# Kernel optimization log

Hardware: AMD Instinct MI355X
Metric: run time of the kernel (lower is better)

Reference implementation:

```python
import jax, jax.numpy as jnp
import numpy as np

NUM_HEADS = 6
ATTN_TH = 0.0
NEG_INF = -10000.0  # masked-score fill for threshold pruning


def setup_inputs() -> dict:
    key = jax.random.key(0)
    k1, k2, k3 = jax.random.split(key, 3)
    B, N, C = 8, 1024, 384
    x = jax.random.normal(k1, (B, N, C), dtype=jnp.float32)
    # Linear weights (torch layout: [out, in]), scaled like default init
    w_qkv = jax.random.normal(k2, (3 * C, C), dtype=jnp.float32) * (1.0 / np.sqrt(C))
    b_qkv = jnp.zeros((3 * C,), dtype=jnp.float32)
    w_proj = jax.random.normal(k3, (C, C), dtype=jnp.float32) * (1.0 / np.sqrt(C))
    b_proj = jnp.zeros((C,), dtype=jnp.float32)
    return {"x": x, "w_qkv": w_qkv, "b_qkv": b_qkv, "w_proj": w_proj, "b_proj": b_proj}


def reference(x, w_qkv, b_qkv, w_proj, b_proj):
    B, N, C = x.shape
    H = NUM_HEADS
    D = C // H
    scale = D ** -0.5
    # QAct nodes are identity (quant=False); QLinear is a plain linear.
    qkv = jnp.einsum('bnc,oc->bno', x, w_qkv) + b_qkv          # [B,N,3C]
    qkv = qkv.reshape(B, N, 3, H, D).transpose(2, 0, 3, 1, 4)   # [3,B,H,N,D]
    q, k, v = qkv[0], qkv[1], qkv[2]
    attn = jnp.einsum('bhnd,bhmd->bhnm', q, k) * scale          # [B,H,N,N]
    # Threshold pruning: scores below Attn_Th are masked out of the softmax.
    attn = jnp.where(attn < ATTN_TH, NEG_INF, attn)
    attn = jax.nn.softmax(attn, axis=-1)
    out = jnp.einsum('bhnm,bhmd->bhnd', attn, v)                # [B,H,N,D]
    out = out.transpose(0, 2, 1, 3).reshape(B, N, C)
    out = jnp.einsum('bnc,oc->bno', out, w_proj) + b_proj
    return out
```

## Files before the change

### kernel.cpp

```cpp
#include <hip/hip_runtime.h>
#include <hip/hip_bf16.h>


typedef __attribute__((__ext_vector_type__(8))) __bf16 bf16x8;
typedef __attribute__((__ext_vector_type__(8))) unsigned short ushort8;
typedef __attribute__((__ext_vector_type__(4))) unsigned short ushort4v;
typedef __attribute__((__ext_vector_type__(4))) short short4v;
typedef __attribute__((__ext_vector_type__(4))) float f32x4;

#define NX 3145728
#define NQ 442368
#define NP 147456

#define QSCALE 0.1803368801111204f

__device__ __forceinline__ f32x4 mfma32(bf16x8 a, bf16x8 b, f32x4 c) {
    return __builtin_amdgcn_mfma_f32_16x16x32_bf16(a, b, c, 0, 0, 0);
}

__device__ __forceinline__ unsigned short f2bf(float f) {
    union { float f; unsigned int i; } x; x.f = f;
    unsigned int u = x.i;
    return (unsigned short)((u + 0x7fffu + ((u >> 16) & 1u)) >> 16);
}

__device__ __forceinline__ unsigned cvtpk(float a, float b) {
    unsigned r;
    asm("v_cvt_pk_bf16_f32 %0, %1, %2" : "=v"(r) : "v"(a), "v"(b));
    return r;
}

__device__ __forceinline__ void dma16(const unsigned short* g, unsigned short* l) {
    __builtin_amdgcn_global_load_lds(
        (const __attribute__((address_space(1))) unsigned int*)g,
        (__attribute__((address_space(3))) unsigned int*)l, 16, 0, 0);
}

__global__ __launch_bounds__(256) void cvt_bf16(
    const float* __restrict__ x, const float* __restrict__ wq, const float* __restrict__ wp,
    unsigned short* __restrict__ xb, unsigned short* __restrict__ wqb, unsigned short* __restrict__ wpb)
{
    int i = blockIdx.x * 256 + threadIdx.x;
    const float* src; unsigned short* dst; int off;
    if (i < NX / 4)              { src = x;  dst = xb;  off = i * 4; }
    else if (i < (NX + NQ) / 4)  { src = wq; dst = wqb; off = i * 4 - NX; }
    else                         { src = wp; dst = wpb; off = i * 4 - NX - NQ; }
    float4 v = *(const float4*)(src + off);
    ushort4v r;
    r[0] = f2bf(v.x); r[1] = f2bf(v.y); r[2] = f2bf(v.z); r[3] = f2bf(v.w);
    *(ushort4v*)(dst + off) = r;
}

template <int MODE, int TM>
__global__ __launch_bounds__(TM * 2) void gemm_bt(
    const unsigned short* __restrict__ A,
    const unsigned short* __restrict__ B,
    const float* __restrict__ bias,
    unsigned short* __restrict__ qg,
    unsigned short* __restrict__ kg,
    unsigned short* __restrict__ vg,
    float* __restrict__ out,
    int M, int N, int K)
{
    const int tid  = threadIdx.x;
    const int lane = tid & 63;
    const int wave = tid >> 6;
    const int l15  = lane & 15;
    const int quad = lane >> 4;
    const int m0 = blockIdx.x * TM;
    const int n0 = blockIdx.y * 128;
    const int wm = (wave >> 1) * 64;
    const int wn = (wave & 1) * 64;

    __shared__ __align__(16) unsigned short As[2 * TM * 32];
    __shared__ __align__(16) unsigned short Bs[2 * 128 * 32];

    f32x4 acc[4][4];
    #pragma unroll
    for (int i = 0; i < 4; ++i)
        #pragma unroll
        for (int j = 0; j < 4; ++j)
            acc[i][j] = (f32x4){0.f, 0.f, 0.f, 0.f};

    auto stage = [&](int k0, int buf) {
        #pragma unroll
        for (int t = 0; t < 2; ++t) {
            int i = tid + t * TM * 2;
            dma16(A + (size_t)(m0 + (i >> 2)) * K + k0 + (i & 3) * 8,
                  As + buf * TM * 32 + t * TM * 16 + wave * 512);
        }
        #pragma unroll
        for (int t = 0; t < 512 / (TM * 2); ++t) {
            int i = tid + t * TM * 2;
            dma16(B + (size_t)(n0 + (i >> 2)) * K + k0 + (i & 3) * 8,
                  Bs + buf * 4096 + t * TM * 16 + wave * 512);
        }
    };

    const int nk = K >> 5;
    stage(0, 0);
    for (int ki = 0; ki < nk; ++ki) {
        __syncthreads();
        if (ki + 1 < nk) stage((ki + 1) << 5, (ki + 1) & 1);
        const unsigned short* as = As + (ki & 1) * TM * 32;
        const unsigned short* bs = Bs + (ki & 1) * 4096;

        bf16x8 af[4], bff[4];
        #pragma unroll
        for (int mt = 0; mt < 4; ++mt)
            af[mt] = *(const bf16x8*)(as + (wm + mt * 16 + l15) * 32 + quad * 8);
        #pragma unroll
        for (int nt = 0; nt < 4; ++nt)
            bff[nt] = *(const bf16x8*)(bs + (wn + nt * 16 + l15) * 32 + quad * 8);
        #pragma unroll
        for (int mt = 0; mt < 4; ++mt)
            #pragma unroll
            for (int nt = 0; nt < 4; ++nt)
                acc[mt][nt] = mfma32(af[mt], bff[nt], acc[mt][nt]);
    }

    if constexpr (MODE == 0) {
        if (n0 < 384) {
            #pragma unroll
            for (int nt = 0; nt < 4; ++nt) {
                int n = n0 + wn + nt * 16 + l15;
                float bv = bias[n];
                #pragma unroll
                for (int mt = 0; mt < 4; ++mt) {
                    int mbase = m0 + wm + mt * 16 + quad * 4;
                    #pragma unroll
                    for (int r = 0; r < 4; ++r)
                        qg[(size_t)(mbase + r) * 384 + n] = f2bf((acc[mt][nt][r] + bv) * QSCALE);
                }
            }
        } else if (n0 < 768) {
            #pragma unroll
            for (int nt = 0; nt < 4; ++nt) {
                int n = n0 + wn + nt * 16 + l15;
                float bv = bias[n];
                int c2 = n - 384;
                int h = c2 >> 6, ck = c2 & 63;
                int half = ck >> 5, qd = (ck >> 3) & 3, j = ck & 7;
                #pragma unroll
                for (int mt = 0; mt < 4; ++mt) {
                    int mbase = m0 + wm + mt * 16 + quad * 4;
                    #pragma unroll
                    for (int r = 0; r < 4; ++r) {
                        int tok = mbase + r;
                        int b = tok >> 10, kv = tok & 1023;
                        int kt = kv >> 4, lk = kv & 15;
                        kg[(size_t)(b * 6 + h) * 65536 +
                           ((((size_t)kt * 2 + half) * 4 + qd) * 16 + lk) * 8 + j]
                            = f2bf(acc[mt][nt][r] + bv);
                    }
                }
            }
        } else {
            #pragma unroll
            for (int nt = 0; nt < 4; ++nt) {
                int n = n0 + wn + nt * 16 + l15;
                float bv = bias[n];
                int c2 = n - 768;
                int h = c2 >> 6, d = c2 & 63;
                int dt = d >> 4, lv = d & 15;
                #pragma unroll
                for (int mt = 0; mt < 4; ++mt) {
                    int mbase = m0 + wm + mt * 16 + quad * 4;
                    int b = mbase >> 10, kvb = mbase & 1023;
                    int cc = kvb >> 6;
                    int hh = (kvb >> 5) & 1;
                    int rem2 = kvb & 31;
                    int qv, j;
                    if (rem2 < 16) { qv = (rem2 >> 3) << 1; j = rem2 & 7; }
                    else {
                        int m2 = rem2 - 16;
                        qv = 1 + ((m2 >> 3) << 1);
                        j = (((m2 >> 2) & 1) ^ 1) << 2;
                    }
                    ushort4v pk;
                    #pragma unroll
                    for (int r = 0; r < 4; ++r) pk[r] = f2bf(acc[mt][nt][r] + bv);
                    *(ushort4v*)(vg + (size_t)(b * 6 + h) * 65536 +
                                 ((((size_t)cc * 2 + hh) * 4 + dt) * 4 + qv) * 128 + lv * 8 + j) = pk;
                }
            }
        }
    } else {
        #pragma unroll
        for (int nt = 0; nt < 4; ++nt) {
            int n = n0 + wn + nt * 16 + l15;
            float bv = bias[n];
            #pragma unroll
            for (int mt = 0; mt < 4; ++mt) {
                int mbase = m0 + wm + mt * 16 + quad * 4;
                #pragma unroll
                for (int r = 0; r < 4; ++r)
                    out[(size_t)(mbase + r) * N + n] = acc[mt][nt][r] + bv;
            }
        }
    }
}

__global__ __launch_bounds__(256) void attn_fused(
    const unsigned short* __restrict__ qg,
    const unsigned short* __restrict__ kg,
    const unsigned short* __restrict__ vg,
    unsigned short* __restrict__ aout)
{
    const int tid  = threadIdx.x;
    const int wave = tid >> 6;
    const int lane = tid & 63;
    const int l15  = lane & 15;
    const int quad = lane >> 4;
    const int id = blockIdx.x;
    const int s  = id % 48;
    const int qt = id / 48;
    const int b  = s / 6;
    const int h  = s % 6;

    const size_t rowbase = (size_t)b * 1024;
    const unsigned short* Kslab = kg + (size_t)s * 65536;
    const unsigned short* Vslab = vg + (size_t)s * 65536;
    const int q0 = qt * 64 + wave * 16;

    __shared__ __align__(16) unsigned short Kb[2 * 4096];
    __shared__ __align__(16) unsigned short Vb[2 * 4096];

    bf16x8 aq0, aq1;
    {
        const unsigned short* qrow = qg + (rowbase + q0 + l15) * 384 + h * 64 + quad * 8;
        aq0 = *(const bf16x8*)qrow;
        aq1 = *(const bf16x8*)(qrow + 32);
    }

    union { unsigned short us[8]; bf16x8 v; } ones_u;
    #pragma unroll
    for (int i = 0; i < 8; ++i) ones_u.us[i] = 0x3F80;
    const bf16x8 ONES8 = ones_u.v;

    f32x4 accO[4];
    #pragma unroll
    for (int dt = 0; dt < 4; ++dt) accO[dt] = (f32x4){0.f, 0.f, 0.f, 0.f};
    f32x4 accS = (f32x4){0.f, 0.f, 0.f, 0.f};

    auto stage = [&](int c, int buf) {
        #pragma unroll
        for (int t = 0; t < 2; ++t) {
            int i = tid + t * 256;
            dma16(Kslab + (size_t)c * 4096 + i * 8, Kb + buf * 4096 + t * 2048 + wave * 512);
            dma16(Vslab + (size_t)c * 4096 + i * 8, Vb + buf * 4096 + t * 2048 + wave * 512);
        }
    };

    const bool oddq = (quad & 1) != 0;

    stage(0, 0);
    for (int c = 0; c < 16; ++c) {
        __syncthreads();
        if (c + 1 < 16) stage(c + 1, (c + 1) & 1);
        const unsigned short* kb = Kb + (c & 1) * 4096;
        const unsigned short* vb = Vb + (c & 1) * 4096;

        #pragma unroll
        for (int hh = 0; hh < 2; ++hh) {
            bf16x8 ka0 = *(const bf16x8*)(kb + (((4 * hh + 0) * 4 + quad) * 16 + l15) * 8);
            bf16x8 ka1 = *(const bf16x8*)(kb + (((4 * hh + 1) * 4 + quad) * 16 + l15) * 8);
            f32x4 za = (f32x4){0.f, 0.f, 0.f, 0.f};
            za = mfma32(ka0, aq0, za);
            za = mfma32(ka1, aq1, za);
            bf16x8 kb0 = *(const bf16x8*)(kb + (((4 * hh + 2) * 4 + quad) * 16 + l15) * 8);
            bf16x8 kb1 = *(const bf16x8*)(kb + (((4 * hh + 3) * 4 + quad) * 16 + l15) * 8);
            f32x4 zb = (f32x4){0.f, 0.f, 0.f, 0.f};
            zb = mfma32(kb0, aq0, zb);
            zb = mfma32(kb1, aq1, zb);

            float ea0 = __builtin_amdgcn_exp2f(za[0]); ea0 = (za[0] < 0.f) ? 0.f : ea0;
            float ea1 = __builtin_amdgcn_exp2f(za[1]); ea1 = (za[1] < 0.f) ? 0.f : ea1;
            float ea2 = __builtin_amdgcn_exp2f(za[2]); ea2 = (za[2] < 0.f) ? 0.f : ea2;
            float ea3 = __builtin_amdgcn_exp2f(za[3]); ea3 = (za[3] < 0.f) ? 0.f : ea3;
            float eb0 = __builtin_amdgcn_exp2f(zb[0]); eb0 = (zb[0] < 0.f) ? 0.f : eb0;
            float eb1 = __builtin_amdgcn_exp2f(zb[1]); eb1 = (zb[1] < 0.f) ? 0.f : eb1;
            float eb2 = __builtin_amdgcn_exp2f(zb[2]); eb2 = (zb[2] < 0.f) ? 0.f : eb2;
            float eb3 = __builtin_amdgcn_exp2f(zb[3]); eb3 = (zb[3] < 0.f) ? 0.f : eb3;

            unsigned A0 = cvtpk(ea0, ea1), A1 = cvtpk(ea2, ea3);
            unsigned B0 = cvtpk(eb0, eb1), B1 = cvtpk(eb2, eb3);

            unsigned send0 = oddq ? A0 : B0, send1 = oddq ? A1 : B1;
            unsigned keep0 = oddq ? B0 : A0, keep1 = oddq ? B1 : A1;
            unsigned rr0 = (unsigned)__shfl_xor((int)send0, 16, 64);
            unsigned rr1 = (unsigned)__shfl_xor((int)send1, 16, 64);

            union { unsigned u[4]; bf16x8 v; } pw;
            pw.u[0] = keep0; pw.u[1] = keep1; pw.u[2] = rr0; pw.u[3] = rr1;

            accS = mfma32(ONES8, pw.v, accS);
            #pragma unroll
            for (int dt = 0; dt < 4; ++dt) {
                bf16x8 vv = *(const bf16x8*)(vb + (((hh * 4 + dt) * 4 + quad) * 16 + l15) * 8);
                accO[dt] = mfma32(vv, pw.v, accO[dt]);
            }
        }
    }

    float inv = 1.0f / accS[0];

    unsigned short* orow = aout + (rowbase + q0 + l15) * 384 + h * 64 + quad * 4;
    #pragma unroll
    for (int dt = 0; dt < 4; ++dt) {
        union { unsigned u[2]; ushort4v s; } pk;
        pk.u[0] = cvtpk(accO[dt][0] * inv, accO[dt][1] * inv);
        pk.u[1] = cvtpk(accO[dt][2] * inv, accO[dt][3] * inv);
        *(ushort4v*)(orow + dt * 16) = pk.s;
    }
}

extern "C" void kernel_launch(void* const* d_in, const int* in_sizes, int n_in,
                              void* d_out, int out_size, void* d_ws, size_t ws_size,
                              hipStream_t stream) {
    const float* x      = (const float*)d_in[0];
    const float* w_qkv  = (const float*)d_in[1];
    const float* b_qkv  = (const float*)d_in[2];
    const float* w_proj = (const float*)d_in[3];
    const float* b_proj = (const float*)d_in[4];
    float* out = (float*)d_out;

    unsigned short* qg   = (unsigned short*)d_ws;
    unsigned short* kgp  = qg   + (size_t)NX;
    unsigned short* vgp  = kgp  + (size_t)NX;
    unsigned short* aout = vgp  + (size_t)NX;
    unsigned short* xb   = aout + (size_t)NX;
    unsigned short* wqb  = xb   + (size_t)NX;
    unsigned short* wpb  = wqb  + (size_t)NQ;

    cvt_bf16<<<3648, 256, 0, stream>>>(x, w_qkv, w_proj, xb, wqb, wpb);
    gemm_bt<0, 256><<<dim3(32, 9), 512, 0, stream>>>(
        xb, wqb, b_qkv, qg, kgp, vgp, nullptr, 8192, 1152, 384);
    attn_fused<<<768, 256, 0, stream>>>(qg, kgp, vgp, aout);
    gemm_bt<1, 64><<<dim3(128, 3), 128, 0, stream>>>(
        aout, wpb, b_proj, nullptr, nullptr, nullptr, out, 8192, 384, 384);
}
```

Baseline: 127.4 us.

## Give each attention wave two query tiles and shrink QKV GEMM tile

The attention kernel now runs 2 waves per block, and each wave processes 32 query rows as two 16-row fragments. The K and V fragments read from shared memory are reused across both fragments, which halves LDS reads per unit of work. Block-level staging is spread over fewer threads, with 4 DMA iterations each. The QKV GEMM also switches to a 128-row tile with 256 threads on a 64x9 grid to get more blocks. In exchange, register pressure per wave rises and there are fewer waves per block to hide staging latency.

```diff
diff --git a/kernel.cpp b/kernel.cpp
--- a/kernel.cpp
+++ b/kernel.cpp
@@ -201,7 +201,7 @@
     }
 }
 
-__global__ __launch_bounds__(256) void attn_fused(
+__global__ __launch_bounds__(128) void attn_fused(
     const unsigned short* __restrict__ qg,
     const unsigned short* __restrict__ kg,
     const unsigned short* __restrict__ vg,
@@ -221,16 +221,19 @@
     const size_t rowbase = (size_t)b * 1024;
     const unsigned short* Kslab = kg + (size_t)s * 65536;
     const unsigned short* Vslab = vg + (size_t)s * 65536;
-    const int q0 = qt * 64 + wave * 16;
+    const int q0 = qt * 64 + wave * 32;
 
     __shared__ __align__(16) unsigned short Kb[2 * 4096];
     __shared__ __align__(16) unsigned short Vb[2 * 4096];
 
-    bf16x8 aq0, aq1;
+    bf16x8 aq0_0, aq1_0, aq0_1, aq1_1;
     {
-        const unsigned short* qrow = qg + (rowbase + q0 + l15) * 384 + h * 64 + quad * 8;
-        aq0 = *(const bf16x8*)qrow;
-        aq1 = *(const bf16x8*)(qrow + 32);
+        const unsigned short* qr0 = qg + (rowbase + q0 + l15) * 384 + h * 64 + quad * 8;
+        aq0_0 = *(const bf16x8*)qr0;
+        aq1_0 = *(const bf16x8*)(qr0 + 32);
+        const unsigned short* qr1 = qr0 + 16 * 384;
+        aq0_1 = *(const bf16x8*)qr1;
+        aq1_1 = *(const bf16x8*)(qr1 + 32);
     }
 
     union { unsigned short us[8]; bf16x8 v; } ones_u;
@@ -238,17 +241,21 @@
     for (int i = 0; i < 8; ++i) ones_u.us[i] = 0x3F80;
     const bf16x8 ONES8 = ones_u.v;
 
-    f32x4 accO[4];
+    f32x4 accO0[4], accO1[4];
     #pragma unroll
-    for (int dt = 0; dt < 4; ++dt) accO[dt] = (f32x4){0.f, 0.f, 0.f, 0.f};
-    f32x4 accS = (f32x4){0.f, 0.f, 0.f, 0.f};
+    for (int dt = 0; dt < 4; ++dt) {
+        accO0[dt] = (f32x4){0.f, 0.f, 0.f, 0.f};
+        accO1[dt] = (f32x4){0.f, 0.f, 0.f, 0.f};
+    }
+    f32x4 accS0 = (f32x4){0.f, 0.f, 0.f, 0.f};
+    f32x4 accS1 = (f32x4){0.f, 0.f, 0.f, 0.f};
 
     auto stage = [&](int c, int buf) {
         #pragma unroll
-        for (int t = 0; t < 2; ++t) {
-            int i = tid + t * 256;
-            dma16(Kslab + (size_t)c * 4096 + i * 8, Kb + buf * 4096 + t * 2048 + wave * 512);
-            dma16(Vslab + (size_t)c * 4096 + i * 8, Vb + buf * 4096 + t * 2048 + wave * 512);
+        for (int t = 0; t < 4; ++t) {
+            int i = tid + t * 128;
+            dma16(Kslab + (size_t)c * 4096 + i * 8, Kb + buf * 4096 + t * 1024 + wave * 512);
+            dma16(Vslab + (size_t)c * 4096 + i * 8, Vb + buf * 4096 + t * 1024 + wave * 512);
         }
     };
 
@@ -265,53 +272,83 @@
         for (int hh = 0; hh < 2; ++hh) {
             bf16x8 ka0 = *(const bf16x8*)(kb + (((4 * hh + 0) * 4 + quad) * 16 + l15) * 8);
             bf16x8 ka1 = *(const bf16x8*)(kb + (((4 * hh + 1) * 4 + quad) * 16 + l15) * 8);
-            f32x4 za = (f32x4){0.f, 0.f, 0.f, 0.f};
-            za = mfma32(ka0, aq0, za);
-            za = mfma32(ka1, aq1, za);
             bf16x8 kb0 = *(const bf16x8*)(kb + (((4 * hh + 2) * 4 + quad) * 16 + l15) * 8);
             bf16x8 kb1 = *(const bf16x8*)(kb + (((4 * hh + 3) * 4 + quad) * 16 + l15) * 8);
-            f32x4 zb = (f32x4){0.f, 0.f, 0.f, 0.f};
-            zb = mfma32(kb0, aq0, zb);
-            zb = mfma32(kb1, aq1, zb);
-
-            float ea0 = __builtin_amdgcn_exp2f(za[0]); ea0 = (za[0] < 0.f) ? 0.f : ea0;
-            float ea1 = __builtin_amdgcn_exp2f(za[1]); ea1 = (za[1] < 0.f) ? 0.f : ea1;
-            float ea2 = __builtin_amdgcn_exp2f(za[2]); ea2 = (za[2] < 0.f) ? 0.f : ea2;
-            float ea3 = __builtin_amdgcn_exp2f(za[3]); ea3 = (za[3] < 0.f) ? 0.f : ea3;
-            float eb0 = __builtin_amdgcn_exp2f(zb[0]); eb0 = (zb[0] < 0.f) ? 0.f : eb0;
-            float eb1 = __builtin_amdgcn_exp2f(zb[1]); eb1 = (zb[1] < 0.f) ? 0.f : eb1;
-            float eb2 = __builtin_amdgcn_exp2f(zb[2]); eb2 = (zb[2] < 0.f) ? 0.f : eb2;
-            float eb3 = __builtin_amdgcn_exp2f(zb[3]); eb3 = (zb[3] < 0.f) ? 0.f : eb3;
-
-            unsigned A0 = cvtpk(ea0, ea1), A1 = cvtpk(ea2, ea3);
-            unsigned B0 = cvtpk(eb0, eb1), B1 = cvtpk(eb2, eb3);
-
-            unsigned send0 = oddq ? A0 : B0, send1 = oddq ? A1 : B1;
-            unsigned keep0 = oddq ? B0 : A0, keep1 = oddq ? B1 : A1;
-            unsigned rr0 = (unsigned)__shfl_xor((int)send0, 16, 64);
-            unsigned rr1 = (unsigned)__shfl_xor((int)send1, 16, 64);
-
-            union { unsigned u[4]; bf16x8 v; } pw;
-            pw.u[0] = keep0; pw.u[1] = keep1; pw.u[2] = rr0; pw.u[3] = rr1;
-
-            accS = mfma32(ONES8, pw.v, accS);
-            #pragma unroll
-            for (int dt = 0; dt < 4; ++dt) {
-                bf16x8 vv = *(const bf16x8*)(vb + (((hh * 4 + dt) * 4 + quad) * 16 + l15) * 8);
-                accO[dt] = mfma32(vv, pw.v, accO[dt]);
-            }
-        }
-    }
-
-    float inv = 1.0f / accS[0];
-
-    unsigned short* orow = aout + (rowbase + q0 + l15) * 384 + h * 64 + quad * 4;
+
+            f32x4 za0 = (f32x4){0.f, 0.f, 0.f, 0.f};
+            za0 = mfma32(ka0, aq0_0, za0);
+            za0 = mfma32(ka1, aq1_0, za0);
+            f32x4 zb0 = (f32x4){0.f, 0.f, 0.f, 0.f};
+            zb0 = mfma32(kb0, aq0_0, zb0);
+            zb0 = mfma32(kb1, aq1_0, zb0);
+            f32x4 za1 = (f32x4){0.f, 0.f, 0.f, 0.f};
+            za1 = mfma32(ka0, aq0_1, za1);
+            za1 = mfma32(ka1, aq1_1, za1);
+            f32x4 zb1 = (f32x4){0.f, 0.f, 0.f, 0.f};
+            zb1 = mfma32(kb0, aq0_1, zb1);
+            zb1 = mfma32(kb1, aq1_1, zb1);
+
+            bf16x8 vv0 = *(const bf16x8*)(vb + (((hh * 4 + 0) * 4 + quad) * 16 + l15) * 8);
+            bf16x8 vv1 = *(const bf16x8*)(vb + (((hh * 4 + 1) * 4 + quad) * 16 + l15) * 8);
+            bf16x8 vv2 = *(const bf16x8*)(vb + (((hh * 4 + 2) * 4 + quad) * 16 + l15) * 8);
+            bf16x8 vv3 = *(const bf16x8*)(vb + (((hh * 4 + 3) * 4 + quad) * 16 + l15) * 8);
+
+            #pragma unroll
+            for (int f = 0; f < 2; ++f) {
+                f32x4 za = f ? za1 : za0;
+                f32x4 zb = f ? zb1 : zb0;
+
+                float ea0 = __builtin_amdgcn_exp2f(za[0]); ea0 = (za[0] < 0.f) ? 0.f : ea0;
+                float ea1 = __builtin_amdgcn_exp2f(za[1]); ea1 = (za[1] < 0.f) ? 0.f : ea1;
+                float ea2 = __builtin_amdgcn_exp2f(za[2]); ea2 = (za[2] < 0.f) ? 0.f : ea2;
+                float ea3 = __builtin_amdgcn_exp2f(za[3]); ea3 = (za[3] < 0.f) ? 0.f : ea3;
+                float eb0 = __builtin_amdgcn_exp2f(zb[0]); eb0 = (zb[0] < 0.f) ? 0.f : eb0;
+                float eb1 = __builtin_amdgcn_exp2f(zb[1]); eb1 = (zb[1] < 0.f) ? 0.f : eb1;
+                float eb2 = __builtin_amdgcn_exp2f(zb[2]); eb2 = (zb[2] < 0.f) ? 0.f : eb2;
+                float eb3 = __builtin_amdgcn_exp2f(zb[3]); eb3 = (zb[3] < 0.f) ? 0.f : eb3;
+
+                unsigned A0 = cvtpk(ea0, ea1), A1 = cvtpk(ea2, ea3);
+                unsigned B0 = cvtpk(eb0, eb1), B1 = cvtpk(eb2, eb3);
+
+                unsigned send0 = oddq ? A0 : B0, send1 = oddq ? A1 : B1;
+                unsigned keep0 = oddq ? B0 : A0, keep1 = oddq ? B1 : A1;
+                unsigned rr0 = (unsigned)__shfl_xor((int)send0, 16, 64);
+                unsigned rr1 = (unsigned)__shfl_xor((int)send1, 16, 64);
+
+                union { unsigned u[4]; bf16x8 v; } pw;
+                pw.u[0] = keep0; pw.u[1] = keep1; pw.u[2] = rr0; pw.u[3] = rr1;
+
+                if (f == 0) {
+                    accS0 = mfma32(ONES8, pw.v, accS0);
+                    accO0[0] = mfma32(vv0, pw.v, accO0[0]);
+                    accO0[1] = mfma32(vv1, pw.v, accO0[1]);
+                    accO0[2] = mfma32(vv2, pw.v, accO0[2]);
+                    accO0[3] = mfma32(vv3, pw.v, accO0[3]);
+                } else {
+                    accS1 = mfma32(ONES8, pw.v, accS1);
+                    accO1[0] = mfma32(vv0, pw.v, accO1[0]);
+                    accO1[1] = mfma32(vv1, pw.v, accO1[1]);
+                    accO1[2] = mfma32(vv2, pw.v, accO1[2]);
+                    accO1[3] = mfma32(vv3, pw.v, accO1[3]);
+                }
+            }
+        }
+    }
+
+    float inv0 = 1.0f / accS0[0];
+    float inv1 = 1.0f / accS1[0];
+
+    unsigned short* orow0 = aout + (rowbase + q0 + l15) * 384 + h * 64 + quad * 4;
+    unsigned short* orow1 = orow0 + 16 * 384;
     #pragma unroll
     for (int dt = 0; dt < 4; ++dt) {
         union { unsigned u[2]; ushort4v s; } pk;
-        pk.u[0] = cvtpk(accO[dt][0] * inv, accO[dt][1] * inv);
-        pk.u[1] = cvtpk(accO[dt][2] * inv, accO[dt][3] * inv);
-        *(ushort4v*)(orow + dt * 16) = pk.s;
+        pk.u[0] = cvtpk(accO0[dt][0] * inv0, accO0[dt][1] * inv0);
+        pk.u[1] = cvtpk(accO0[dt][2] * inv0, accO0[dt][3] * inv0);
+        *(ushort4v*)(orow0 + dt * 16) = pk.s;
+        pk.u[0] = cvtpk(accO1[dt][0] * inv1, accO1[dt][1] * inv1);
+        pk.u[1] = cvtpk(accO1[dt][2] * inv1, accO1[dt][3] * inv1);
+        *(ushort4v*)(orow1 + dt * 16) = pk.s;
     }
 }
 
@@ -334,9 +371,9 @@
     unsigned short* wpb  = wqb  + (size_t)NQ;
 
     cvt_bf16<<<3648, 256, 0, stream>>>(x, w_qkv, w_proj, xb, wqb, wpb);
-    gemm_bt<0, 256><<<dim3(32, 9), 512, 0, stream>>>(
+    gemm_bt<0, 128><<<dim3(64, 9), 256, 0, stream>>>(
         xb, wqb, b_qkv, qg, kgp, vgp, nullptr, 8192, 1152, 384);
-    attn_fused<<<768, 256, 0, stream>>>(qg, kgp, vgp, aout);
+    attn_fused<<<768, 128, 0, stream>>>(qg, kgp, vgp, aout);
     gemm_bt<1, 64><<<dim3(128, 3), 128, 0, stream>>>(
         aout, wpb, b_proj, nullptr, nullptr, nullptr, out, 8192, 384, 384);
 }
```

Result: slower. 143.0 us (+12.2%).

## Triple-buffer LDS staging with explicit vmcnt waits and shrink QKV GEMM tile

Applied to the files above, without the earlier changes.

The GEMM and attention kernels now use three LDS buffers with a prefetch distance of two K-chunks. Explicit s_waitcnt vmcnt counts followed by a raw s_barrier replace __syncthreads, so the loads for the next chunk can stay in flight while the current one is computed. The QKV projection GEMM also moves from a 256-row tile with 512 threads to a 128-row tile with 256 threads, doubling the grid. This adds LDS per block, which may reduce occupancy, and relies on the hand-set vmcnt values matching the exact number of DMA loads issued per stage.

```diff
diff --git a/kernel.cpp b/kernel.cpp
--- a/kernel.cpp
+++ b/kernel.cpp
@@ -72,8 +72,8 @@
     const int wm = (wave >> 1) * 64;
     const int wn = (wave & 1) * 64;
 
-    __shared__ __align__(16) unsigned short As[2 * TM * 32];
-    __shared__ __align__(16) unsigned short Bs[2 * 128 * 32];
+    __shared__ __align__(16) unsigned short As[3 * TM * 32];
+    __shared__ __align__(16) unsigned short Bs[3 * 128 * 32];
 
     f32x4 acc[4][4];
     #pragma unroll
@@ -97,13 +97,24 @@
         }
     };
 
+    constexpr int S = 2 + 512 / (TM * 2);
     const int nk = K >> 5;
     stage(0, 0);
+    stage(32, 1);
     for (int ki = 0; ki < nk; ++ki) {
-        __syncthreads();
-        if (ki + 1 < nk) stage((ki + 1) << 5, (ki + 1) & 1);
-        const unsigned short* as = As + (ki & 1) * TM * 32;
-        const unsigned short* bs = Bs + (ki & 1) * 4096;
+        if (ki + 1 < nk) {
+            if constexpr (S == 3)      asm volatile("s_waitcnt vmcnt(3) lgkmcnt(0)" ::: "memory");
+            else if constexpr (S == 4) asm volatile("s_waitcnt vmcnt(4) lgkmcnt(0)" ::: "memory");
+            else                       asm volatile("s_waitcnt vmcnt(6) lgkmcnt(0)" ::: "memory");
+        } else {
+            asm volatile("s_waitcnt vmcnt(0) lgkmcnt(0)" ::: "memory");
+        }
+        __builtin_amdgcn_s_barrier();
+        __builtin_amdgcn_sched_barrier(0);
+        if (ki + 2 < nk) stage((ki + 2) << 5, (ki + 2) % 3);
+
+        const unsigned short* as = As + (ki % 3) * TM * 32;
+        const unsigned short* bs = Bs + (ki % 3) * 4096;
 
         bf16x8 af[4], bff[4];
         #pragma unroll
@@ -223,8 +234,8 @@
     const unsigned short* Vslab = vg + (size_t)s * 65536;
     const int q0 = qt * 64 + wave * 16;
 
-    __shared__ __align__(16) unsigned short Kb[2 * 4096];
-    __shared__ __align__(16) unsigned short Vb[2 * 4096];
+    __shared__ __align__(16) unsigned short Kb[3 * 4096];
+    __shared__ __align__(16) unsigned short Vb[3 * 4096];
 
     bf16x8 aq0, aq1;
     {
@@ -255,11 +266,16 @@
     const bool oddq = (quad & 1) != 0;
 
     stage(0, 0);
+    stage(1, 1);
     for (int c = 0; c < 16; ++c) {
-        __syncthreads();
-        if (c + 1 < 16) stage(c + 1, (c + 1) & 1);
-        const unsigned short* kb = Kb + (c & 1) * 4096;
-        const unsigned short* vb = Vb + (c & 1) * 4096;
+        if (c < 15) asm volatile("s_waitcnt vmcnt(4) lgkmcnt(0)" ::: "memory");
+        else        asm volatile("s_waitcnt vmcnt(0) lgkmcnt(0)" ::: "memory");
+        __builtin_amdgcn_s_barrier();
+        __builtin_amdgcn_sched_barrier(0);
+        if (c + 2 < 16) stage(c + 2, (c + 2) % 3);
+
+        const unsigned short* kb = Kb + (c % 3) * 4096;
+        const unsigned short* vb = Vb + (c % 3) * 4096;
 
         #pragma unroll
         for (int hh = 0; hh < 2; ++hh) {
@@ -334,7 +350,7 @@
     unsigned short* wpb  = wqb  + (size_t)NQ;
 
     cvt_bf16<<<3648, 256, 0, stream>>>(x, w_qkv, w_proj, xb, wqb, wpb);
-    gemm_bt<0, 256><<<dim3(32, 9), 512, 0, stream>>>(
+    gemm_bt<0, 128><<<dim3(64, 9), 256, 0, stream>>>(
         xb, wqb, b_qkv, qg, kgp, vgp, nullptr, 8192, 1152, 384);
     attn_fused<<<768, 256, 0, stream>>>(qg, kgp, vgp, aout);
     gemm_bt<1, 64><<<dim3(128, 3), 128, 0, stream>>>(
```

New measurement: 133.5 us. 1.05x slower.
